# Kernel tuning notes

Measured on AMD Instinct MI355X. Metric: run time of the kernel, lower is better.

The kernel has to match this reference:

```python
import jax, jax.numpy as jnp
import numpy as np

D_MODEL = 1024
N_LAYER = 4
VOCAB = 50288  # 50277 padded to multiple of 16
D_STATE = 128
D_CONV = 4
HEADDIM = 64
CHUNK = 64
D_INNER = 2 * D_MODEL            # expand=2 -> 2048
NHEADS = D_INNER // HEADDIM      # 32
D_IN_PROJ = 2 * D_INNER + 2 * D_STATE + NHEADS  # ngroups=1
CONV_DIM = D_INNER + 2 * D_STATE
BATCH = 1
SEQLEN = 1024
EPS = 1e-5


def silu(x):
    return x * jax.nn.sigmoid(x)


def rmsnorm(x, w, z=None):
    if z is not None:
        x = x * silu(z)
    return x * jax.lax.rsqrt(jnp.mean(x * x, axis=-1, keepdims=True) + EPS) * w


def segsum(x):
    # x: (..., T) -> (..., T, T) with segment sums below diagonal, -inf above
    T = x.shape[-1]
    xe = jnp.broadcast_to(x[..., None], x.shape + (T,))
    mask_lo = jnp.tril(jnp.ones((T, T), dtype=bool), -1)
    xe = jnp.where(mask_lo, xe, 0.0)
    s = jnp.cumsum(xe, axis=-2)
    mask = jnp.tril(jnp.ones((T, T), dtype=bool), 0)
    return jnp.where(mask, s, -jnp.inf)


def ssd(x, dt, A, B, C, Dp):
    # x: (b,s,h,p), dt/A-broadcast: (b,s,h), B/C: (b,s,n) (ngroups=1), Dp: (h,)
    b, s = x.shape[0], x.shape[1]
    nchunks = s // CHUNK
    xD = x * Dp[:, None]
    Adt = A * dt                      # (b,s,h)
    xdt = x * dt[..., None]
    xr = xdt.reshape(b, nchunks, CHUNK, NHEADS, HEADDIM)
    Ar = Adt.reshape(b, nchunks, CHUNK, NHEADS).transpose(0, 3, 1, 2)  # (b,h,c,l)
    Br = B.reshape(b, nchunks, CHUNK, D_STATE)
    Cr = C.reshape(b, nchunks, CHUNK, D_STATE)
    A_cumsum = jnp.cumsum(Ar, axis=-1)                  # (b,h,c,l)
    L = jnp.exp(segsum(Ar))                             # (b,h,c,l,l)
    Y_diag = jnp.einsum('bcln,bcsn,bhcls,bcshp->bclhp', Cr, Br, L, xr)
    decay_states = jnp.exp(A_cumsum[..., -1:] - A_cumsum)
    states = jnp.einsum('bcln,bhcl,bclhp->bchpn', Br, decay_states, xr)
    states = jnp.concatenate([jnp.zeros_like(states[:, :1]), states], axis=1)
    decay_chunk = jnp.exp(segsum(jnp.pad(A_cumsum[..., -1], ((0, 0), (0, 0), (1, 0)))))
    new_states = jnp.einsum('bhzc,bchpn->bzhpn', decay_chunk, states)
    states = new_states[:, :-1]
    state_decay_out = jnp.exp(A_cumsum)
    Y_off = jnp.einsum('bcln,bchpn,bhcl->bclhp', Cr, states, state_decay_out)
    Y = (Y_diag + Y_off).reshape(b, s, NHEADS, HEADDIM) + xD
    return Y


def mamba2_forward(input_ids, embedding, norm_w, in_proj_w, conv_w, conv_b,
                   dt_bias, A_log, D, mixer_norm_w, out_proj_w, norm_f_w):
    h = embedding[input_ids]  # (b,s,d_model)
    for l in range(N_LAYER):
        u = rmsnorm(h, norm_w[l])
        zxbcdt = u @ in_proj_w[l].T  # (b,s,d_in_proj)
        z = zxbcdt[..., :D_INNER]
        xBC = zxbcdt[..., D_INNER:D_INNER + CONV_DIM]
        dt = jax.nn.softplus(zxbcdt[..., -NHEADS:] + dt_bias[l])
        # causal depthwise conv1d
        xc = jnp.transpose(xBC, (0, 2, 1))
        xc = jax.lax.conv_general_dilated(
            xc, conv_w[l], (1,), [(D_CONV - 1, 0)],
            dimension_numbers=('NCH', 'OIH', 'NCH'),
            feature_group_count=CONV_DIM) + conv_b[l][None, :, None]
        xBC = silu(jnp.transpose(xc, (0, 2, 1)))
        x = xBC[..., :D_INNER].reshape(BATCH, SEQLEN, NHEADS, HEADDIM)
        B = xBC[..., D_INNER:D_INNER + D_STATE]
        C = xBC[..., D_INNER + D_STATE:]
        A = -jnp.exp(A_log[l])  # (h,)
        y = ssd(x, dt, A, B, C, D[l])
        y = rmsnorm(y.reshape(BATCH, SEQLEN, D_INNER), mixer_norm_w[l], z)
        h = h + y @ out_proj_w[l].T
    h = rmsnorm(h, norm_f_w)
    return h @ embedding.T  # tied lm_head


def setup_inputs() -> dict:
    key = jax.random.key(0)
    ks = jax.random.split(key, 10)
    def rn(k, shape, s=0.02):
        return jax.random.normal(k, shape, jnp.float32) * s
    return {
        'input_ids': jax.random.randint(ks[0], (BATCH, SEQLEN), 0, VOCAB, jnp.int32),
        'embedding': rn(ks[1], (VOCAB, D_MODEL)),
        'norm_w': jnp.ones((N_LAYER, D_MODEL), jnp.float32),
        'in_proj_w': rn(ks[2], (N_LAYER, D_IN_PROJ, D_MODEL)),
        'conv_w': rn(ks[3], (N_LAYER, CONV_DIM, 1, D_CONV), 0.2),
        'conv_b': jnp.zeros((N_LAYER, CONV_DIM), jnp.float32),
        'dt_bias': rn(ks[4], (N_LAYER, NHEADS), 0.5),
        'A_log': jnp.log(jax.random.uniform(ks[5], (N_LAYER, NHEADS), jnp.float32, 1.0, 16.0)),
        'D': jnp.ones((N_LAYER, NHEADS), jnp.float32) + rn(ks[6], (N_LAYER, NHEADS), 0.1),
        'mixer_norm_w': jnp.ones((N_LAYER, D_INNER), jnp.float32),
        'out_proj_w': rn(ks[7], (N_LAYER, D_MODEL, D_INNER)),
        'norm_f_w': jnp.ones((D_MODEL,), jnp.float32),
    }


def reference(input_ids, embedding, norm_w, in_proj_w, conv_w, conv_b,
              dt_bias, A_log, D, mixer_norm_w, out_proj_w, norm_f_w):
    return mamba2_forward(input_ids, embedding, norm_w, in_proj_w, conv_w, conv_b,
                          dt_bias, A_log, D, mixer_norm_w, out_proj_w, norm_f_w)
```

## Files before the change

### kernel.cpp

```cpp
#include <hip/hip_runtime.h>
#include <hip/hip_bf16.h>
#include <math.h>

#define D_MODEL   1024
#define VOCAB     50288
#define D_STATE   128
#define D_CONV    4
#define HEADDIM   64
#define CHUNK     64
#define D_INNER   2048
#define NHEADS    32
#define D_IN_PROJ 4384
#define CONV_DIM  2304
#define SEQ       1024
#define NCHUNKS   16
#define EPS       1e-5f
#define SZH       1048576

typedef __bf16 bf16x8 __attribute__((ext_vector_type(8)));
typedef __bf16 bf16x4 __attribute__((ext_vector_type(4)));
typedef float  f32x4  __attribute__((ext_vector_type(4)));

__device__ __forceinline__ float blockReduceSum256(float v, float* sm) {
    #pragma unroll
    for (int off = 32; off > 0; off >>= 1) v += __shfl_down(v, off);
    if ((threadIdx.x & 63) == 0) sm[threadIdx.x >> 6] = v;
    __syncthreads();
    return sm[0] + sm[1] + sm[2] + sm[3];
}

__device__ __forceinline__ float sigmoidf_(float x) { return 1.0f / (1.0f + expf(-x)); }

__device__ __forceinline__ void gload_lds16(const __bf16* g, __bf16* l) {
    __builtin_amdgcn_global_load_lds(
        (const __attribute__((address_space(1))) void*)g,
        (__attribute__((address_space(3))) void*)l,
        16, 0, 0);
}

__global__ void cvt_bf16_k(const float* __restrict__ src, __bf16* __restrict__ dst, long n) {
    long i = ((long)blockIdx.x * 256 + threadIdx.x) * 8;
    long stride = (long)gridDim.x * 256 * 8;
    for (; i < n; i += stride) {
        float4 a = *(const float4*)(src + i);
        float4 b = *(const float4*)(src + i + 4);
        bf16x8 o;
        o[0] = (__bf16)a.x; o[1] = (__bf16)a.y; o[2] = (__bf16)a.z; o[3] = (__bf16)a.w;
        o[4] = (__bf16)b.x; o[5] = (__bf16)b.y; o[6] = (__bf16)b.z; o[7] = (__bf16)b.w;
        *(bf16x8*)(dst + i) = o;
    }
}

__global__ void gather_k(const int* __restrict__ ids, const float* __restrict__ emb,
                         float* __restrict__ h) {
    int s = blockIdx.x;
    int id = ids[s];
    const float4* src = (const float4*)(emb + (size_t)id * D_MODEL);
    float4* dst = (float4*)(h + (size_t)s * D_MODEL);
    dst[threadIdx.x] = src[threadIdx.x];
}

__global__ void rmsnorm_k(const float* __restrict__ x, const float* __restrict__ w,
                          float* __restrict__ o) {
    __shared__ float red[4];
    int s = blockIdx.x, t = threadIdx.x;
    float4 v = ((const float4*)(x + (size_t)s * D_MODEL))[t];
    float ss = v.x*v.x + v.y*v.y + v.z*v.z + v.w*v.w;
    float tot = blockReduceSum256(ss, red);
    float r = rsqrtf(tot / (float)D_MODEL + EPS);
    float4 wv = ((const float4*)w)[t];
    float4 ov;
    ov.x = v.x * r * wv.x; ov.y = v.y * r * wv.y;
    ov.z = v.z * r * wv.z; ov.w = v.w * r * wv.w;
    ((float4*)(o + (size_t)s * D_MODEL))[t] = ov;
}

__global__ void rmsnorm_fold_bf16_k(float* __restrict__ h, const float* __restrict__ o,
                                    const float* __restrict__ w, __bf16* __restrict__ out) {
    __shared__ float red[4];
    int s = blockIdx.x, t = threadIdx.x;
    float4 v = ((const float4*)(h + (size_t)s * D_MODEL))[t];
    if (o) {
        #pragma unroll
        for (int j = 0; j < 4; ++j) {
            float4 ov = ((const float4*)(o + (size_t)j * SZH + (size_t)s * D_MODEL))[t];
            v.x += ov.x; v.y += ov.y; v.z += ov.z; v.w += ov.w;
        }
        ((float4*)(h + (size_t)s * D_MODEL))[t] = v;
    }
    float ss = v.x*v.x + v.y*v.y + v.z*v.z + v.w*v.w;
    float tot = blockReduceSum256(ss, red);
    float r = rsqrtf(tot / (float)D_MODEL + EPS);
    float4 wv = ((const float4*)w)[t];
    bf16x4 ov;
    ov[0] = (__bf16)(v.x * r * wv.x); ov[1] = (__bf16)(v.y * r * wv.y);
    ov[2] = (__bf16)(v.z * r * wv.z); ov[3] = (__bf16)(v.w * r * wv.w);
    *(bf16x4*)(out + (size_t)s * D_MODEL + t * 4) = ov;
}

__global__ void gatednorm_k(float* __restrict__ Y, const float* __restrict__ zx,
                            const float* __restrict__ w) {
    __shared__ float red[4];
    int s = blockIdx.x, t = threadIdx.x;
    float4 y0 = ((const float4*)(Y + (size_t)s * D_INNER))[2*t];
    float4 y1 = ((const float4*)(Y + (size_t)s * D_INNER))[2*t+1];
    float4 z0 = ((const float4*)(zx + (size_t)s * D_IN_PROJ))[2*t];
    float4 z1 = ((const float4*)(zx + (size_t)s * D_IN_PROJ))[2*t+1];
    float g[8];
    float yv[8] = { y0.x,y0.y,y0.z,y0.w, y1.x,y1.y,y1.z,y1.w };
    float zv[8] = { z0.x,z0.y,z0.z,z0.w, z1.x,z1.y,z1.z,z1.w };
    float ss = 0.f;
    #pragma unroll
    for (int j = 0; j < 8; ++j) {
        float gg = yv[j] * zv[j] * sigmoidf_(zv[j]);
        g[j] = gg;
        ss += gg * gg;
    }
    float tot = blockReduceSum256(ss, red);
    float r = rsqrtf(tot / (float)D_INNER + EPS);
    float4 o0, o1;
    o0.x = g[0]*r*w[8*t+0]; o0.y = g[1]*r*w[8*t+1]; o0.z = g[2]*r*w[8*t+2]; o0.w = g[3]*r*w[8*t+3];
    o1.x = g[4]*r*w[8*t+4]; o1.y = g[5]*r*w[8*t+5]; o1.z = g[6]*r*w[8*t+6]; o1.w = g[7]*r*w[8*t+7];
    ((float4*)(Y + (size_t)s * D_INNER))[2*t]   = o0;
    ((float4*)(Y + (size_t)s * D_INNER))[2*t+1] = o1;
}

__global__ void gatednorm_bf16_k(const float* __restrict__ Y, const float* __restrict__ zx0,
                                 const float* __restrict__ zx1,
                                 const float* __restrict__ w, __bf16* __restrict__ o) {
    __shared__ float red[4];
    int s = blockIdx.x, t = threadIdx.x;
    float4 y0 = ((const float4*)(Y + (size_t)s * D_INNER))[2*t];
    float4 y1 = ((const float4*)(Y + (size_t)s * D_INNER))[2*t+1];
    float4 z0 = ((const float4*)(zx0 + (size_t)s * D_IN_PROJ))[2*t];
    float4 z1 = ((const float4*)(zx0 + (size_t)s * D_IN_PROJ))[2*t+1];
    if (zx1) {
        float4 a0 = ((const float4*)(zx1 + (size_t)s * D_IN_PROJ))[2*t];
        float4 a1 = ((const float4*)(zx1 + (size_t)s * D_IN_PROJ))[2*t+1];
        z0.x += a0.x; z0.y += a0.y; z0.z += a0.z; z0.w += a0.w;
        z1.x += a1.x; z1.y += a1.y; z1.z += a1.z; z1.w += a1.w;
    }
    float g[8];
    float yv[8] = { y0.x,y0.y,y0.z,y0.w, y1.x,y1.y,y1.z,y1.w };
    float zv[8] = { z0.x,z0.y,z0.z,z0.w, z1.x,z1.y,z1.z,z1.w };
    float ss = 0.f;
    #pragma unroll
    for (int j = 0; j < 8; ++j) {
        float gg = yv[j] * zv[j] * sigmoidf_(zv[j]);
        g[j] = gg;
        ss += gg * gg;
    }
    float tot = blockReduceSum256(ss, red);
    float r = rsqrtf(tot / (float)D_INNER + EPS);
    bf16x8 ov;
    #pragma unroll
    for (int j = 0; j < 8; ++j) ov[j] = (__bf16)(g[j] * r * w[8*t+j]);
    *(bf16x8*)(o + (size_t)s * D_INNER + t * 8) = ov;
}

template<int TM, int TN, int MTL2, bool ACC>
__global__ __launch_bounds__(256) void gemm_bt_bf16(const __bf16* __restrict__ A,
                                                    const __bf16* __restrict__ B,
                                                    float* __restrict__ C,
                                                    int N, int klen,
                                                    int lda, int ldb, int ldc,
                                                    int ntiles, size_t csplit) {
    constexpr int FM = TM / 32;
    constexpr int FN = TN / 32;
    __shared__ __bf16 As[TM * 32];
    __shared__ __bf16 Bs[TN * 32];

    const int d = blockIdx.x;
    const int xcd = d & 7;
    const int kk = d >> 3;
    const int p = kk >> MTL2;
    const int m_tile = kk & ((1 << MTL2) - 1);
    const int n_tile = xcd + (p << 3);
    if (n_tile >= ntiles) return;

    const int k_begin = blockIdx.y * klen;
    C += (size_t)blockIdx.y * csplit;

    const int bm0 = m_tile * TM;
    const int bn0 = n_tile * TN;
    const int t = threadIdx.x;
    const int l = t & 63;
    const int w = t >> 6;
    const int wr = w >> 1, wc = w & 1;
    const int lrow = l & 15;
    const int lk   = (l >> 4) * 8;
    const int srow = l >> 2;
    const int scol = (l & 3) * 8;

    f32x4 acc[FM][FN];
    #pragma unroll
    for (int m = 0; m < FM; ++m)
        #pragma unroll
        for (int n = 0; n < FN; ++n)
            acc[m][n] = (f32x4){0.f, 0.f, 0.f, 0.f};

    for (int k0 = k_begin; k0 < k_begin + klen; k0 += 32) {
        __syncthreads();
        #pragma unroll
        for (int i = 0; i < TM / 64; ++i) {
            int r0 = w * (TM / 4) + i * 16;
            const __bf16* g = A + (size_t)(bm0 + r0 + srow) * lda + k0 + scol;
            gload_lds16(g, As + (size_t)r0 * 32);
        }
        #pragma unroll
        for (int i = 0; i < TN / 64; ++i) {
            int r0 = w * (TN / 4) + i * 16;
            int gn = bn0 + r0 + srow; if (gn > N - 1) gn = N - 1;
            const __bf16* g = B + (size_t)gn * ldb + k0 + scol;
            gload_lds16(g, Bs + (size_t)r0 * 32);
        }
        __syncthreads();

        bf16x8 af[FM], bfr[FN];
        #pragma unroll
        for (int m = 0; m < FM; ++m)
            af[m] = *(const bf16x8*)&As[(wr * (TM/2) + m * 16 + lrow) * 32 + lk];
        #pragma unroll
        for (int n = 0; n < FN; ++n)
            bfr[n] = *(const bf16x8*)&Bs[(wc * (TN/2) + n * 16 + lrow) * 32 + lk];
        #pragma unroll
        for (int m = 0; m < FM; ++m)
            #pragma unroll
            for (int n = 0; n < FN; ++n)
                acc[m][n] = __builtin_amdgcn_mfma_f32_16x16x32_bf16(af[m], bfr[n], acc[m][n], 0, 0, 0);
    }

    const int r0 = (l >> 4) * 4;
    #pragma unroll
    for (int m = 0; m < FM; ++m) {
        #pragma unroll
        for (int rr = 0; rr < 4; ++rr) {
            int gr = bm0 + wr * (TM/2) + m * 16 + r0 + rr;
            #pragma unroll
            for (int n = 0; n < FN; ++n) {
                int gc = bn0 + wc * (TN/2) + n * 16 + lrow;
                if (gc < N) {
                    size_t off = (size_t)gr * ldc + gc;
                    if (ACC) C[off] += acc[m][n][rr];
                    else     C[off]  = acc[m][n][rr];
                }
            }
        }
    }
}

template<bool ACC>
__global__ __launch_bounds__(256) void gemm_nt_cvt(const float* __restrict__ A,
                                                   const float* __restrict__ B,
                                                   float* __restrict__ C,
                                                   int M, int N, int K,
                                                   int lda, int ldb, int ldc) {
    __shared__ __bf16 As[128][40];
    __shared__ __bf16 Bs[128][40];
    const int bm0 = blockIdx.x * 128;
    const int bn0 = blockIdx.y * 128;
    const int t = threadIdx.x;
    const int l = t & 63;
    const int w = t >> 6;
    const int wr = w >> 1;
    const int wc = w & 1;
    const int lrow = l & 15;
    const int lk   = (l >> 4) * 8;

    f32x4 acc[4][4];
    #pragma unroll
    for (int m = 0; m < 4; ++m)
        #pragma unroll
        for (int n = 0; n < 4; ++n)
            acc[m][n] = (f32x4){0.f, 0.f, 0.f, 0.f};

    for (int k0 = 0; k0 < K; k0 += 32) {
        __syncthreads();
        float4 av[4], bv[4];
        #pragma unroll
        for (int i = 0; i < 4; ++i) {
            int idx = t + i * 256;
            int r = idx >> 3;
            int c4 = (idx & 7) * 4;
            av[i] = *(const float4*)(A + (size_t)(bm0 + r) * lda + k0 + c4);
            int gn = bn0 + r; if (gn > N - 1) gn = N - 1;
            bv[i] = *(const float4*)(B + (size_t)gn * ldb + k0 + c4);
        }
        #pragma unroll
        for (int i = 0; i < 4; ++i) {
            int idx = t + i * 256;
            int r = idx >> 3;
            int c4 = (idx & 7) * 4;
            bf16x4 aw, bw;
            aw[0] = (__bf16)av[i].x; aw[1] = (__bf16)av[i].y;
            aw[2] = (__bf16)av[i].z; aw[3] = (__bf16)av[i].w;
            bw[0] = (__bf16)bv[i].x; bw[1] = (__bf16)bv[i].y;
            bw[2] = (__bf16)bv[i].z; bw[3] = (__bf16)bv[i].w;
            *(bf16x4*)&As[r][c4] = aw;
            *(bf16x4*)&Bs[r][c4] = bw;
        }
        __syncthreads();

        bf16x8 af[4], bfr[4];
        #pragma unroll
        for (int m = 0; m < 4; ++m)
            af[m] = *(const bf16x8*)&As[wr * 64 + m * 16 + lrow][lk];
        #pragma unroll
        for (int n = 0; n < 4; ++n)
            bfr[n] = *(const bf16x8*)&Bs[wc * 64 + n * 16 + lrow][lk];
        #pragma unroll
        for (int m = 0; m < 4; ++m)
            #pragma unroll
            for (int n = 0; n < 4; ++n)
                acc[m][n] = __builtin_amdgcn_mfma_f32_16x16x32_bf16(af[m], bfr[n], acc[m][n], 0, 0, 0);
    }

    const int r0 = (l >> 4) * 4;
    #pragma unroll
    for (int m = 0; m < 4; ++m) {
        #pragma unroll
        for (int rr = 0; rr < 4; ++rr) {
            int gr = bm0 + wr * 64 + m * 16 + r0 + rr;
            #pragma unroll
            for (int n = 0; n < 4; ++n) {
                int gc = bn0 + wc * 64 + n * 16 + lrow;
                if (gc < N) {
                    size_t off = (size_t)gr * ldc + gc;
                    if (ACC) C[off] += acc[m][n][rr];
                    else     C[off]  = acc[m][n][rr];
                }
            }
        }
    }
}

__global__ void conv_silu_k(const float* __restrict__ zx0, const float* __restrict__ zx1,
                            const float* __restrict__ w,
                            const float* __restrict__ b, float* __restrict__ xBC) {
    int idx = blockIdx.x * 256 + threadIdx.x;
    if (idx >= SEQ * CONV_DIM) return;
    int s = idx / CONV_DIM, c = idx - s * CONV_DIM;
    float acc = b[c];
    #pragma unroll
    for (int k = 0; k < D_CONV; ++k) {
        int si = s + k - (D_CONV - 1);
        if (si >= 0) {
            size_t o = (size_t)si * D_IN_PROJ + D_INNER + c;
            float v = zx0[o];
            if (zx1) v += zx1[o];
            acc = fmaf(v, w[c * D_CONV + k], acc);
        }
    }
    xBC[idx] = acc * sigmoidf_(acc);
}

__global__ void dtcum_k(const float* __restrict__ zx0, const float* __restrict__ zx1,
                        const float* __restrict__ dt_bias,
                        const float* __restrict__ A_log,
                        float* __restrict__ dtb, float* __restrict__ acs) {
    int c = blockIdx.x, h = blockIdx.y, l = threadIdx.x;
    int s = c * 64 + l;
    size_t o = (size_t)s * D_IN_PROJ + (D_IN_PROJ - NHEADS) + h;
    float v = zx0[o];
    if (zx1) v += zx1[o];
    v += dt_bias[h];
    float dt = (v > 20.f) ? v : log1pf(expf(v));
    dtb[(size_t)s * NHEADS + h] = dt;
    float a = -expf(A_log[h]);
    float x = a * dt;
    #pragma unroll
    for (int off = 1; off < 64; off <<= 1) {
        float oo = __shfl_up(x, off);
        if (l >= off) x += oo;
    }
    acs[(size_t)h * SEQ + s] = x;
}

__global__ __launch_bounds__(256) void chunk_cm_k(const float* __restrict__ xBC,
                                                  float* __restrict__ cm) {
    int c = blockIdx.x, g = blockIdx.y;
    __shared__ float Cs[16][D_STATE];
    __shared__ float BsT[D_STATE][64];
    int t = threadIdx.x;
    #pragma unroll
    for (int i = 0; i < 2; ++i) {
        int idx = t + i * 256;
        int li = idx >> 5, n4 = (idx & 31) * 4;
        *(float4*)&Cs[li][n4] =
            *(const float4*)(xBC + (size_t)(c*64 + g*16 + li) * CONV_DIM + D_INNER + D_STATE + n4);
    }
    #pragma unroll
    for (int i = 0; i < 8; ++i) {
        int idx = t + i * 256;
        int sx = idx & 63, n4 = (idx >> 6) * 4;
        float4 v = *(const float4*)(xBC + (size_t)(c*64 + sx) * CONV_DIM + D_INNER + n4);
        BsT[n4+0][sx] = v.x; BsT[n4+1][sx] = v.y; BsT[n4+2][sx] = v.z; BsT[n4+3][sx] = v.w;
    }
    __syncthreads();
    #pragma unroll
    for (int i = 0; i < 4; ++i) {
        int e = t + i * 256;
        int li = e >> 6, sx = e & 63;
        int l = g * 16 + li;
        float d = 0.f;
        if (sx <= l) {
            #pragma unroll 8
            for (int n = 0; n < D_STATE; ++n) d = fmaf(Cs[li][n], BsT[n][sx], d);
        }
        cm[(size_t)c * 4096 + l * 64 + sx] = d;
    }
}

__global__ __launch_bounds__(256) void ydst_k(const float* __restrict__ cm,
                                              const float* __restrict__ xBC,
                                              const float* __restrict__ dtb,
                                              const float* __restrict__ acs,
                                              float* __restrict__ Y,
                                              float* __restrict__ st) {
    int c = blockIdx.x, h = blockIdx.y;
    __shared__ float Xs[64][64];
    __shared__ float Us[64][128];
    __shared__ float arow[64];
    __shared__ float dec[64];
    int t = threadIdx.x;
    if (t < 64) arow[t] = acs[(size_t)h * SEQ + c * 64 + t];
    __syncthreads();
    float alast = arow[63];
    if (t < 64) dec[t] = expf(alast - arow[t]);
    #pragma unroll
    for (int i = 0; i < 4; ++i) {
        int idx = t + i * 256;
        int l = idx >> 4, p4 = (idx & 15) * 4;
        int s = c * 64 + l;
        float4 v = *(const float4*)(xBC + (size_t)s * CONV_DIM + h * HEADDIM + p4);
        float d = dtb[(size_t)s * NHEADS + h];
        v.x *= d; v.y *= d; v.z *= d; v.w *= d;
        *(float4*)&Xs[l][p4] = v;
    }
    #pragma unroll
    for (int i = 0; i < 16; ++i) {
        int e = t + i * 256;
        int l = e >> 6, sx = e & 63;
        Us[l][sx] = (sx <= l) ? cm[(size_t)c * 4096 + e] * expf(arow[l] - arow[sx]) : 0.f;
    }
    __syncthreads();
    #pragma unroll
    for (int i = 0; i < 4; ++i) {
        int e = t + i * 256;
        int l = e >> 4, p4 = (e & 15) * 4;
        float ax = 0.f, ay = 0.f, az = 0.f, aw = 0.f;
        for (int sx = 0; sx <= l; ++sx) {
            float gg = Us[l][sx];
            float4 xv = *(const float4*)&Xs[sx][p4];
            ax = fmaf(gg, xv.x, ax); ay = fmaf(gg, xv.y, ay);
            az = fmaf(gg, xv.z, az); aw = fmaf(gg, xv.w, aw);
        }
        float4 ov; ov.x = ax; ov.y = ay; ov.z = az; ov.w = aw;
        *(float4*)(Y + (size_t)(c*64 + l) * D_INNER + h * HEADDIM + p4) = ov;
    }
    __syncthreads();
    #pragma unroll
    for (int i = 0; i < 8; ++i) {
        int idx = t + i * 256;
        int l = idx >> 5, n4 = (idx & 31) * 4;
        *(float4*)&Us[l][n4] =
            *(const float4*)(xBC + (size_t)(c*64 + l) * CONV_DIM + D_INNER + n4);
    }
    __syncthreads();
    #pragma unroll
    for (int i = 0; i < 8; ++i) {
        int e = t + i * 256;
        int n = e >> 4, p4 = (e & 15) * 4;
        float ax = 0.f, ay = 0.f, az = 0.f, aw = 0.f;
        #pragma unroll 4
        for (int l = 0; l < 64; ++l) {
            float bd = Us[l][n] * dec[l];
            float4 xv = *(const float4*)&Xs[l][p4];
            ax = fmaf(bd, xv.x, ax); ay = fmaf(bd, xv.y, ay);
            az = fmaf(bd, xv.z, az); aw = fmaf(bd, xv.w, aw);
        }
        float4 ov; ov.x = ax; ov.y = ay; ov.z = az; ov.w = aw;
        *(float4*)(st + ((size_t)(c * NHEADS + h) * D_STATE + n) * HEADDIM + p4) = ov;
    }
}

__global__ void rec_k(float* __restrict__ st, const float* __restrict__ acs) {
    int idx = blockIdx.x * 256 + threadIdx.x;
    int h = idx >> 13;
    float S = 0.f;
    for (int c = 0; c < NCHUNKS; ++c) {
        float* p = st + (size_t)c * (NHEADS * D_STATE * HEADDIM) + idx;
        float tmp = *p;
        *p = S;
        float dec = expf(acs[(size_t)h * SEQ + c * 64 + 63]);
        S = fmaf(S, dec, tmp);
    }
}

__global__ __launch_bounds__(256) void yoff_k(const float* __restrict__ xBC,
                                              const float* __restrict__ acs,
                                              const float* __restrict__ st,
                                              const float* __restrict__ Dp,
                                              float* __restrict__ Y) {
    int c = blockIdx.x, h = blockIdx.y;
    __shared__ float Cs[64][D_STATE];
    __shared__ float Ss[D_STATE][64];
    __shared__ float arow[64];
    int t = threadIdx.x;
    if (t < 64) arow[t] = acs[(size_t)h * SEQ + c * 64 + t];
    #pragma unroll
    for (int i = 0; i < 8; ++i) {
        int idx = t + i * 256;
        int l = idx >> 5, n4 = (idx & 31) * 4;
        *(float4*)&Cs[l][n4] =
            *(const float4*)(xBC + (size_t)(c*64 + l) * CONV_DIM + D_INNER + D_STATE + n4);
    }
    #pragma unroll
    for (int i = 0; i < 8; ++i) {
        int idx = t + i * 256;
        int n = idx >> 4, p4 = (idx & 15) * 4;
        *(float4*)&Ss[n][p4] =
            *(const float4*)(st + ((size_t)(c * NHEADS + h) * D_STATE + n) * HEADDIM + p4);
    }
    __syncthreads();
    float dpar = Dp[h];
    #pragma unroll
    for (int i = 0; i < 4; ++i) {
        int e = t + i * 256;
        int l = e >> 4, p4 = (e & 15) * 4;
        float ax = 0.f, ay = 0.f, az = 0.f, aw = 0.f;
        #pragma unroll 4
        for (int n = 0; n < D_STATE; ++n) {
            float cc = Cs[l][n];
            float4 sv = *(const float4*)&Ss[n][p4];
            ax = fmaf(cc, sv.x, ax); ay = fmaf(cc, sv.y, ay);
            az = fmaf(cc, sv.z, az); aw = fmaf(cc, sv.w, aw);
        }
        float sc = expf(arow[l]);
        int s = c * 64 + l;
        float4 xv = *(const float4*)(xBC + (size_t)s * CONV_DIM + h * HEADDIM + p4);
        float4 yv = *(float4*)(Y + (size_t)s * D_INNER + h * HEADDIM + p4);
        yv.x += sc * ax + dpar * xv.x;
        yv.y += sc * ay + dpar * xv.y;
        yv.z += sc * az + dpar * xv.z;
        yv.w += sc * aw + dpar * xv.w;
        *(float4*)(Y + (size_t)s * D_INNER + h * HEADDIM + p4) = yv;
    }
}

extern "C" void kernel_launch(void* const* d_in, const int* in_sizes, int n_in,
                              void* d_out, int out_size, void* d_ws, size_t ws_size,
                              hipStream_t stream) {
    const int*   ids          = (const int*)d_in[0];
    const float* emb          = (const float*)d_in[1];
    const float* norm_w       = (const float*)d_in[2];
    const float* in_proj_w    = (const float*)d_in[3];
    const float* conv_w       = (const float*)d_in[4];
    const float* conv_b       = (const float*)d_in[5];
    const float* dt_bias      = (const float*)d_in[6];
    const float* A_log        = (const float*)d_in[7];
    const float* Dp           = (const float*)d_in[8];
    const float* mixer_norm_w = (const float*)d_in[9];
    const float* out_proj_w   = (const float*)d_in[10];
    const float* norm_f_w     = (const float*)d_in[11];
    float* out = (float*)d_out;

    const size_t SZ_H = SZH, SZ_U = SZH, SZ_ZX = 4489216, SZ_XBC = 2359296,
                 SZ_DT = 32768, SZ_ACS = 32768, SZ_CM = 65536, SZ_ST = 4194304, SZ_Y = 2097152;
    const size_t BF_U = SZ_H, BF_Y = SZ_Y;
    const size_t BF_WIN  = 4ull * 4489216;
    const size_t BF_WOUT = 4ull * 2097152;
    const size_t BF_EMB  = (size_t)VOCAB * D_MODEL;

    const size_t f32_base = SZ_H + SZ_U + SZ_ZX + SZ_XBC + SZ_DT + SZ_ACS + SZ_CM + SZ_ST + SZ_Y;
    const size_t f32_new  = f32_base + SZ_ZX + 4 * SZ_H;
    const size_t bf_all   = (BF_U + BF_Y + BF_WIN + BF_WOUT + BF_EMB) * 2;
    const size_t bytesNew = f32_new * 4 + bf_all;
    const size_t bytesOld = f32_base * 4 + bf_all;
    const int tier = (ws_size >= bytesNew) ? 0 : (ws_size >= bytesOld) ? 1 : 2;

    float *h, *u, *dtb, *acs, *cm, *zx, *zxb = nullptr, *xBC, *st, *Y, *o = nullptr;
    __bf16 *ub = nullptr, *Yb = nullptr, *win = nullptr, *wout = nullptr, *embb = nullptr;

    if (tier <= 1) {
        float* f = (float*)d_ws;
        h = f;   f += SZ_H;
        u = f;   f += SZ_U;
        dtb = f; f += SZ_DT;
        acs = f; f += SZ_ACS;
        cm = f;  f += SZ_CM;
        zx = f;  f += SZ_ZX;
        if (tier == 0) {
            zxb = f; f += SZ_ZX;
            o = f;   f += 4 * SZ_H;
        }
        xBC = f; f += SZ_XBC;
        st = f;  f += SZ_ST;
        Y = f;   f += SZ_Y;
        __bf16* bb = (__bf16*)f;
        ub = bb;   bb += BF_U;
        Yb = bb;   bb += BF_Y;
        win = bb;  bb += BF_WIN;
        wout = bb; bb += BF_WOUT;
        embb = bb;
    } else {
        float* f = (float*)d_ws;
        h = f;   f += SZ_H;
        u = f;   f += SZ_U;
        dtb = f; f += SZ_DT;
        acs = f; f += SZ_ACS;
        cm = f;  f += SZ_CM;
        float* ob = (float*)d_out;
        zx = ob;
        xBC = zx + SZ_ZX;
        st = xBC + SZ_XBC;
        Y = st + SZ_ST;
    }

    if (tier <= 1) {
        cvt_bf16_k<<<(int)(BF_WIN / 2048), 256, 0, stream>>>(in_proj_w, win, (long)BF_WIN);
        cvt_bf16_k<<<(int)(BF_WOUT / 2048), 256, 0, stream>>>(out_proj_w, wout, (long)BF_WOUT);
        cvt_bf16_k<<<(int)(BF_EMB / 2048), 256, 0, stream>>>(emb, embb, (long)BF_EMB);
    }

    gather_k<<<SEQ, 256, 0, stream>>>(ids, emb, h);

    const int NT_IN  = (D_IN_PROJ + 127) / 128;
    const int NT_OUT = D_MODEL / 128;
    const int NT_LM  = (VOCAB + 127) / 128;
    const int GX_IN  = 8 * ((NT_IN  + 7) / 8) * 8;
    const int GX_OUT = 8 * ((NT_OUT + 7) / 8) * 16;
    const int GX_LM  = 8 * ((NT_LM  + 7) / 8) * 8;

    for (int l = 0; l < 4; ++l) {
        if (tier <= 1) {
            rmsnorm_fold_bf16_k<<<SEQ, 256, 0, stream>>>(
                h, (tier == 0 && l > 0) ? o : nullptr, norm_w + (size_t)l * D_MODEL, ub);
            if (tier == 0) {
                gemm_bt_bf16<128, 128, 3, false><<<dim3(GX_IN, 2), 256, 0, stream>>>(
                    ub, win + (size_t)l * 4489216, zx,
                    D_IN_PROJ, 512, D_MODEL, D_MODEL, D_IN_PROJ, NT_IN, SZ_ZX);
            } else {
                gemm_bt_bf16<128, 128, 3, false><<<dim3(GX_IN, 1), 256, 0, stream>>>(
                    ub, win + (size_t)l * 4489216, zx,
                    D_IN_PROJ, 1024, D_MODEL, D_MODEL, D_IN_PROJ, NT_IN, 0);
            }
        } else {
            rmsnorm_k<<<SEQ, 256, 0, stream>>>(h, norm_w + (size_t)l * D_MODEL, u);
            gemm_nt_cvt<false><<<dim3(8, 35), 256, 0, stream>>>(
                u, in_proj_w + (size_t)l * D_IN_PROJ * D_MODEL, zx,
                SEQ, D_IN_PROJ, D_MODEL, D_MODEL, D_MODEL, D_IN_PROJ);
        }

        float* zx1 = (tier == 0) ? zxb : nullptr;

        conv_silu_k<<<(SEQ * CONV_DIM) / 256, 256, 0, stream>>>(
            zx, zx1, conv_w + (size_t)l * CONV_DIM * D_CONV, conv_b + (size_t)l * CONV_DIM, xBC);

        dtcum_k<<<dim3(NCHUNKS, NHEADS), 64, 0, stream>>>(
            zx, zx1, dt_bias + (size_t)l * NHEADS, A_log + (size_t)l * NHEADS, dtb, acs);

        chunk_cm_k<<<dim3(NCHUNKS, 4), 256, 0, stream>>>(xBC, cm);

        ydst_k<<<dim3(NCHUNKS, NHEADS), 256, 0, stream>>>(cm, xBC, dtb, acs, Y, st);

        rec_k<<<(NHEADS * D_STATE * HEADDIM) / 256, 256, 0, stream>>>(st, acs);

        yoff_k<<<dim3(NCHUNKS, NHEADS), 256, 0, stream>>>(xBC, acs, st, Dp + (size_t)l * NHEADS, Y);

        if (tier <= 1) {
            gatednorm_bf16_k<<<SEQ, 256, 0, stream>>>(Y, zx, zx1, mixer_norm_w + (size_t)l * D_INNER, Yb);
            if (tier == 0) {
                gemm_bt_bf16<64, 128, 4, false><<<dim3(GX_OUT, 4), 256, 0, stream>>>(
                    Yb, wout + (size_t)l * 2097152, o,
                    D_MODEL, 512, D_INNER, D_INNER, D_MODEL, NT_OUT, SZ_H);
            } else {
                gemm_bt_bf16<64, 128, 4, true><<<dim3(GX_OUT, 1), 256, 0, stream>>>(
                    Yb, wout + (size_t)l * 2097152, h,
                    D_MODEL, 2048, D_INNER, D_INNER, D_MODEL, NT_OUT, 0);
            }
        } else {
            gatednorm_k<<<SEQ, 256, 0, stream>>>(Y, zx, mixer_norm_w + (size_t)l * D_INNER);
            gemm_nt_cvt<true><<<dim3(8, 8), 256, 0, stream>>>(
                Y, out_proj_w + (size_t)l * D_MODEL * D_INNER, h,
                SEQ, D_MODEL, D_INNER, D_INNER, D_INNER, D_MODEL);
        }
    }

    if (tier <= 1) {
        rmsnorm_fold_bf16_k<<<SEQ, 256, 0, stream>>>(
            h, (tier == 0) ? o : nullptr, norm_f_w, ub);
        gemm_bt_bf16<128, 128, 3, false><<<dim3(GX_LM, 1), 256, 0, stream>>>(
            ub, embb, out, VOCAB, 1024, D_MODEL, D_MODEL, VOCAB, NT_LM, 0);
    } else {
        rmsnorm_k<<<SEQ, 256, 0, stream>>>(h, norm_f_w, u);
        gemm_nt_cvt<false><<<dim3(8, (VOCAB + 127) / 128), 256, 0, stream>>>(
            u, emb, out, SEQ, VOCAB, D_MODEL, D_MODEL, D_MODEL, VOCAB);
    }
}
```

Before: 826.6 us.

## Move SSD chunk matmuls to bf16 MFMA with pre-transposed B buffer

Rewrites the chunk C·B^T, intra-chunk Y_diag, chunk-state and Y_off computations to use 16x16x32 bf16 MFMA instructions instead of scalar fp32 FMA loops. The B operand is converted to bf16 and transposed once per chunk into a new global buffer that the per-head kernel reuses. The decay factor is folded into a second scaled copy of x, and the state layout changes to (p, n) order. This cuts the scalar FMA work in these kernels but adds bf16 rounding in the SSD path and a new workspace buffer.

```diff
diff --git a/kernel.cpp b/kernel.cpp
--- a/kernel.cpp
+++ b/kernel.cpp
@@ -376,111 +376,162 @@
     acs[(size_t)h * SEQ + s] = x;
 }
 
-__global__ __launch_bounds__(256) void chunk_cm_k(const float* __restrict__ xBC,
-                                                  float* __restrict__ cm) {
-    int c = blockIdx.x, g = blockIdx.y;
-    __shared__ float Cs[16][D_STATE];
-    __shared__ float BsT[D_STATE][64];
-    int t = threadIdx.x;
-    #pragma unroll
-    for (int i = 0; i < 2; ++i) {
-        int idx = t + i * 256;
-        int li = idx >> 5, n4 = (idx & 31) * 4;
-        *(float4*)&Cs[li][n4] =
-            *(const float4*)(xBC + (size_t)(c*64 + g*16 + li) * CONV_DIM + D_INNER + D_STATE + n4);
-    }
+__global__ __launch_bounds__(256) void cmg_k(const float* __restrict__ xBC,
+                                             float* __restrict__ cm,
+                                             __bf16* __restrict__ btg) {
+    const int c = blockIdx.x;
+    const int LDP = 136;
+    __shared__ __bf16 Cs[64 * 136];
+    __shared__ __bf16 Bs[64 * 136];
+    const int t = threadIdx.x;
+    const int l = t & 63;
+    const int w = t >> 6;
+
     #pragma unroll
     for (int i = 0; i < 8; ++i) {
-        int idx = t + i * 256;
-        int sx = idx & 63, n4 = (idx >> 6) * 4;
-        float4 v = *(const float4*)(xBC + (size_t)(c*64 + sx) * CONV_DIM + D_INNER + n4);
-        BsT[n4+0][sx] = v.x; BsT[n4+1][sx] = v.y; BsT[n4+2][sx] = v.z; BsT[n4+3][sx] = v.w;
+        int e = t + i * 256;
+        int row = e >> 5, n4 = (e & 31) * 4;
+        float4 vc = *(const float4*)(xBC + (size_t)(c*64 + row) * CONV_DIM + D_INNER + D_STATE + n4);
+        float4 vb = *(const float4*)(xBC + (size_t)(c*64 + row) * CONV_DIM + D_INNER + n4);
+        bf16x4 cc, bb;
+        cc[0] = (__bf16)vc.x; cc[1] = (__bf16)vc.y; cc[2] = (__bf16)vc.z; cc[3] = (__bf16)vc.w;
+        bb[0] = (__bf16)vb.x; bb[1] = (__bf16)vb.y; bb[2] = (__bf16)vb.z; bb[3] = (__bf16)vb.w;
+        *(bf16x4*)&Cs[row * LDP + n4] = cc;
+        *(bf16x4*)&Bs[row * LDP + n4] = bb;
     }
     __syncthreads();
+
     #pragma unroll
     for (int i = 0; i < 4; ++i) {
-        int e = t + i * 256;
-        int li = e >> 6, sx = e & 63;
-        int l = g * 16 + li;
-        float d = 0.f;
-        if (sx <= l) {
-            #pragma unroll 8
-            for (int n = 0; n < D_STATE; ++n) d = fmaf(Cs[li][n], BsT[n][sx], d);
-        }
-        cm[(size_t)c * 4096 + l * 64 + sx] = d;
-    }
+        int e8 = t + i * 256;
+        int n = e8 >> 3, l8 = (e8 & 7) * 8;
+        bf16x8 o;
+        #pragma unroll
+        for (int j = 0; j < 8; ++j) o[j] = Bs[(l8 + j) * LDP + n];
+        *(bf16x8*)(btg + ((size_t)c * 128 + n) * 64 + l8) = o;
+    }
+
+    const int lrow = l & 15;
+    const int lk   = (l >> 4) * 8;
+    const int l0 = w * 16;
+    f32x4 acc[4];
+    #pragma unroll
+    for (int n = 0; n < 4; ++n) acc[n] = (f32x4){0.f,0.f,0.f,0.f};
+    #pragma unroll
+    for (int kc = 0; kc < 4; ++kc) {
+        bf16x8 a = *(const bf16x8*)&Cs[(l0 + lrow) * LDP + kc * 32 + lk];
+        #pragma unroll
+        for (int n = 0; n < 4; ++n) {
+            bf16x8 b = *(const bf16x8*)&Bs[(n * 16 + lrow) * LDP + kc * 32 + lk];
+            acc[n] = __builtin_amdgcn_mfma_f32_16x16x32_bf16(a, b, acc[n], 0, 0, 0);
+        }
+    }
+    const int r0 = (l >> 4) * 4;
+    #pragma unroll
+    for (int n = 0; n < 4; ++n)
+        #pragma unroll
+        for (int r = 0; r < 4; ++r)
+            cm[(size_t)c * 4096 + (l0 + r0 + r) * 64 + n * 16 + lrow] = acc[n][r];
 }
 
 __global__ __launch_bounds__(256) void ydst_k(const float* __restrict__ cm,
+                                              const __bf16* __restrict__ btg,
                                               const float* __restrict__ xBC,
                                               const float* __restrict__ dtb,
                                               const float* __restrict__ acs,
                                               float* __restrict__ Y,
                                               float* __restrict__ st) {
-    int c = blockIdx.x, h = blockIdx.y;
-    __shared__ float Xs[64][64];
-    __shared__ float Us[64][128];
+    const int c = blockIdx.x, h = blockIdx.y;
+    const int LDP = 72;
+    __shared__ __bf16 Xt[64 * 72];
+    __shared__ __bf16 X2[64 * 72];
+    __shared__ __bf16 G [64 * 72];
+    __shared__ __bf16 Bt[128 * 72];
     __shared__ float arow[64];
-    __shared__ float dec[64];
-    int t = threadIdx.x;
+    __shared__ float decl[64];
+    const int t = threadIdx.x;
+    const int l = t & 63;
+    const int w = t >> 6;
+
     if (t < 64) arow[t] = acs[(size_t)h * SEQ + c * 64 + t];
     __syncthreads();
-    float alast = arow[63];
-    if (t < 64) dec[t] = expf(alast - arow[t]);
+    const float alast = arow[63];
+    if (t < 64) decl[t] = expf(alast - arow[t]);
+    #pragma unroll
+    for (int i = 0; i < 16; ++i) {
+        int e = t + i * 256;
+        int gl = e >> 6, sx = e & 63;
+        G[gl * LDP + sx] = (sx <= gl) ? (__bf16)(cm[(size_t)c * 4096 + e] * expf(arow[gl] - arow[sx])) : (__bf16)0.f;
+    }
     #pragma unroll
     for (int i = 0; i < 4; ++i) {
-        int idx = t + i * 256;
-        int l = idx >> 4, p4 = (idx & 15) * 4;
-        int s = c * 64 + l;
+        int e8 = t + i * 256;
+        int n = e8 >> 3, l8 = (e8 & 7) * 8;
+        *(bf16x8*)&Bt[n * LDP + l8] = *(const bf16x8*)(btg + ((size_t)c * 128 + n) * 64 + l8);
+    }
+    __syncthreads();
+    #pragma unroll
+    for (int i = 0; i < 4; ++i) {
+        int e4 = t + i * 256;
+        int sx = e4 >> 4, p4 = (e4 & 15) * 4;
+        int s = c * 64 + sx;
         float4 v = *(const float4*)(xBC + (size_t)s * CONV_DIM + h * HEADDIM + p4);
         float d = dtb[(size_t)s * NHEADS + h];
-        v.x *= d; v.y *= d; v.z *= d; v.w *= d;
-        *(float4*)&Xs[l][p4] = v;
-    }
-    #pragma unroll
-    for (int i = 0; i < 16; ++i) {
-        int e = t + i * 256;
-        int l = e >> 6, sx = e & 63;
-        Us[l][sx] = (sx <= l) ? cm[(size_t)c * 4096 + e] * expf(arow[l] - arow[sx]) : 0.f;
+        float d2 = d * decl[sx];
+        Xt[(p4+0) * LDP + sx] = (__bf16)(v.x * d);
+        Xt[(p4+1) * LDP + sx] = (__bf16)(v.y * d);
+        Xt[(p4+2) * LDP + sx] = (__bf16)(v.z * d);
+        Xt[(p4+3) * LDP + sx] = (__bf16)(v.w * d);
+        X2[(p4+0) * LDP + sx] = (__bf16)(v.x * d2);
+        X2[(p4+1) * LDP + sx] = (__bf16)(v.y * d2);
+        X2[(p4+2) * LDP + sx] = (__bf16)(v.z * d2);
+        X2[(p4+3) * LDP + sx] = (__bf16)(v.w * d2);
     }
     __syncthreads();
-    #pragma unroll
-    for (int i = 0; i < 4; ++i) {
-        int e = t + i * 256;
-        int l = e >> 4, p4 = (e & 15) * 4;
-        float ax = 0.f, ay = 0.f, az = 0.f, aw = 0.f;
-        for (int sx = 0; sx <= l; ++sx) {
-            float gg = Us[l][sx];
-            float4 xv = *(const float4*)&Xs[sx][p4];
-            ax = fmaf(gg, xv.x, ax); ay = fmaf(gg, xv.y, ay);
-            az = fmaf(gg, xv.z, az); aw = fmaf(gg, xv.w, aw);
-        }
-        float4 ov; ov.x = ax; ov.y = ay; ov.z = az; ov.w = aw;
-        *(float4*)(Y + (size_t)(c*64 + l) * D_INNER + h * HEADDIM + p4) = ov;
-    }
-    __syncthreads();
-    #pragma unroll
-    for (int i = 0; i < 8; ++i) {
-        int idx = t + i * 256;
-        int l = idx >> 5, n4 = (idx & 31) * 4;
-        *(float4*)&Us[l][n4] =
-            *(const float4*)(xBC + (size_t)(c*64 + l) * CONV_DIM + D_INNER + n4);
-    }
-    __syncthreads();
-    #pragma unroll
-    for (int i = 0; i < 8; ++i) {
-        int e = t + i * 256;
-        int n = e >> 4, p4 = (e & 15) * 4;
-        float ax = 0.f, ay = 0.f, az = 0.f, aw = 0.f;
-        #pragma unroll 4
-        for (int l = 0; l < 64; ++l) {
-            float bd = Us[l][n] * dec[l];
-            float4 xv = *(const float4*)&Xs[l][p4];
-            ax = fmaf(bd, xv.x, ax); ay = fmaf(bd, xv.y, ay);
-            az = fmaf(bd, xv.z, az); aw = fmaf(bd, xv.w, aw);
-        }
-        float4 ov; ov.x = ax; ov.y = ay; ov.z = az; ov.w = aw;
-        *(float4*)(st + ((size_t)(c * NHEADS + h) * D_STATE + n) * HEADDIM + p4) = ov;
+
+    const int lrow = l & 15;
+    const int lk   = (l >> 4) * 8;
+    const int p0 = w * 16;
+    const int r0 = (l >> 4) * 4;
+
+    f32x4 acc1[4];
+    #pragma unroll
+    for (int n = 0; n < 4; ++n) acc1[n] = (f32x4){0.f,0.f,0.f,0.f};
+    #pragma unroll
+    for (int kc = 0; kc < 2; ++kc) {
+        bf16x8 a = *(const bf16x8*)&Xt[(p0 + lrow) * LDP + kc * 32 + lk];
+        #pragma unroll
+        for (int n = 0; n < 4; ++n) {
+            bf16x8 b = *(const bf16x8*)&G[(n * 16 + lrow) * LDP + kc * 32 + lk];
+            acc1[n] = __builtin_amdgcn_mfma_f32_16x16x32_bf16(a, b, acc1[n], 0, 0, 0);
+        }
+    }
+    #pragma unroll
+    for (int n = 0; n < 4; ++n) {
+        int lc = n * 16 + lrow;
+        float4 ov; ov.x = acc1[n][0]; ov.y = acc1[n][1]; ov.z = acc1[n][2]; ov.w = acc1[n][3];
+        *(float4*)(Y + (size_t)(c*64 + lc) * D_INNER + h * HEADDIM + p0 + r0) = ov;
+    }
+
+    f32x4 acc2[8];
+    #pragma unroll
+    for (int n = 0; n < 8; ++n) acc2[n] = (f32x4){0.f,0.f,0.f,0.f};
+    #pragma unroll
+    for (int kc = 0; kc < 2; ++kc) {
+        bf16x8 a = *(const bf16x8*)&X2[(p0 + lrow) * LDP + kc * 32 + lk];
+        #pragma unroll
+        for (int n = 0; n < 8; ++n) {
+            bf16x8 b = *(const bf16x8*)&Bt[(n * 16 + lrow) * LDP + kc * 32 + lk];
+            acc2[n] = __builtin_amdgcn_mfma_f32_16x16x32_bf16(a, b, acc2[n], 0, 0, 0);
+        }
+    }
+    float* stb = st + ((size_t)(c * NHEADS + h) * 64) * 128;
+    #pragma unroll
+    for (int n = 0; n < 8; ++n) {
+        int nc = n * 16 + lrow;
+        #pragma unroll
+        for (int r = 0; r < 4; ++r)
+            stb[(size_t)(p0 + r0 + r) * 128 + nc] = acc2[n][r];
     }
 }
 
@@ -502,49 +553,61 @@
                                               const float* __restrict__ st,
                                               const float* __restrict__ Dp,
                                               float* __restrict__ Y) {
-    int c = blockIdx.x, h = blockIdx.y;
-    __shared__ float Cs[64][D_STATE];
-    __shared__ float Ss[D_STATE][64];
+    const int c = blockIdx.x, h = blockIdx.y;
+    const int LDP = 136;
+    __shared__ __bf16 Sts[64 * 136];
+    __shared__ __bf16 Cs [64 * 136];
     __shared__ float arow[64];
-    int t = threadIdx.x;
+    const int t = threadIdx.x;
+    const int l = t & 63;
+    const int w = t >> 6;
+
     if (t < 64) arow[t] = acs[(size_t)h * SEQ + c * 64 + t];
+    const float* stb = st + ((size_t)(c * NHEADS + h) * 64) * 128;
     #pragma unroll
     for (int i = 0; i < 8; ++i) {
-        int idx = t + i * 256;
-        int l = idx >> 5, n4 = (idx & 31) * 4;
-        *(float4*)&Cs[l][n4] =
-            *(const float4*)(xBC + (size_t)(c*64 + l) * CONV_DIM + D_INNER + D_STATE + n4);
-    }
-    #pragma unroll
-    for (int i = 0; i < 8; ++i) {
-        int idx = t + i * 256;
-        int n = idx >> 4, p4 = (idx & 15) * 4;
-        *(float4*)&Ss[n][p4] =
-            *(const float4*)(st + ((size_t)(c * NHEADS + h) * D_STATE + n) * HEADDIM + p4);
+        int e = t + i * 256;
+        int row = e >> 5, n4 = (e & 31) * 4;
+        float4 vs = *(const float4*)(stb + (size_t)row * 128 + n4);
+        float4 vc = *(const float4*)(xBC + (size_t)(c*64 + row) * CONV_DIM + D_INNER + D_STATE + n4);
+        bf16x4 ss, cc;
+        ss[0] = (__bf16)vs.x; ss[1] = (__bf16)vs.y; ss[2] = (__bf16)vs.z; ss[3] = (__bf16)vs.w;
+        cc[0] = (__bf16)vc.x; cc[1] = (__bf16)vc.y; cc[2] = (__bf16)vc.z; cc[3] = (__bf16)vc.w;
+        *(bf16x4*)&Sts[row * LDP + n4] = ss;
+        *(bf16x4*)&Cs [row * LDP + n4] = cc;
     }
     __syncthreads();
-    float dpar = Dp[h];
-    #pragma unroll
-    for (int i = 0; i < 4; ++i) {
-        int e = t + i * 256;
-        int l = e >> 4, p4 = (e & 15) * 4;
-        float ax = 0.f, ay = 0.f, az = 0.f, aw = 0.f;
-        #pragma unroll 4
-        for (int n = 0; n < D_STATE; ++n) {
-            float cc = Cs[l][n];
-            float4 sv = *(const float4*)&Ss[n][p4];
-            ax = fmaf(cc, sv.x, ax); ay = fmaf(cc, sv.y, ay);
-            az = fmaf(cc, sv.z, az); aw = fmaf(cc, sv.w, aw);
-        }
-        float sc = expf(arow[l]);
-        int s = c * 64 + l;
-        float4 xv = *(const float4*)(xBC + (size_t)s * CONV_DIM + h * HEADDIM + p4);
-        float4 yv = *(float4*)(Y + (size_t)s * D_INNER + h * HEADDIM + p4);
-        yv.x += sc * ax + dpar * xv.x;
-        yv.y += sc * ay + dpar * xv.y;
-        yv.z += sc * az + dpar * xv.z;
-        yv.w += sc * aw + dpar * xv.w;
-        *(float4*)(Y + (size_t)s * D_INNER + h * HEADDIM + p4) = yv;
+
+    const int lrow = l & 15;
+    const int lk   = (l >> 4) * 8;
+    const int p0 = w * 16;
+    const int r0 = (l >> 4) * 4;
+    const float dpar = Dp[h];
+
+    f32x4 acc[4];
+    #pragma unroll
+    for (int n = 0; n < 4; ++n) acc[n] = (f32x4){0.f,0.f,0.f,0.f};
+    #pragma unroll
+    for (int kc = 0; kc < 4; ++kc) {
+        bf16x8 a = *(const bf16x8*)&Sts[(p0 + lrow) * LDP + kc * 32 + lk];
+        #pragma unroll
+        for (int n = 0; n < 4; ++n) {
+            bf16x8 b = *(const bf16x8*)&Cs[(n * 16 + lrow) * LDP + kc * 32 + lk];
+            acc[n] = __builtin_amdgcn_mfma_f32_16x16x32_bf16(a, b, acc[n], 0, 0, 0);
+        }
+    }
+    #pragma unroll
+    for (int n = 0; n < 4; ++n) {
+        int lc = n * 16 + lrow;
+        int s = c * 64 + lc;
+        float sc = expf(arow[lc]);
+        float4 xv = *(const float4*)(xBC + (size_t)s * CONV_DIM + h * HEADDIM + p0 + r0);
+        float4 yv = *(float4*)(Y + (size_t)s * D_INNER + h * HEADDIM + p0 + r0);
+        yv.x += sc * acc[n][0] + dpar * xv.x;
+        yv.y += sc * acc[n][1] + dpar * xv.y;
+        yv.z += sc * acc[n][2] + dpar * xv.z;
+        yv.w += sc * acc[n][3] + dpar * xv.w;
+        *(float4*)(Y + (size_t)s * D_INNER + h * HEADDIM + p0 + r0) = yv;
     }
 }
 
@@ -567,12 +630,13 @@
 
     const size_t SZ_H = SZH, SZ_U = SZH, SZ_ZX = 4489216, SZ_XBC = 2359296,
                  SZ_DT = 32768, SZ_ACS = 32768, SZ_CM = 65536, SZ_ST = 4194304, SZ_Y = 2097152;
+    const size_t SZ_BTG_F = 65536;
     const size_t BF_U = SZ_H, BF_Y = SZ_Y;
     const size_t BF_WIN  = 4ull * 4489216;
     const size_t BF_WOUT = 4ull * 2097152;
     const size_t BF_EMB  = (size_t)VOCAB * D_MODEL;
 
-    const size_t f32_base = SZ_H + SZ_U + SZ_ZX + SZ_XBC + SZ_DT + SZ_ACS + SZ_CM + SZ_ST + SZ_Y;
+    const size_t f32_base = SZ_H + SZ_U + SZ_ZX + SZ_XBC + SZ_DT + SZ_ACS + SZ_CM + SZ_BTG_F + SZ_ST + SZ_Y;
     const size_t f32_new  = f32_base + SZ_ZX + 4 * SZ_H;
     const size_t bf_all   = (BF_U + BF_Y + BF_WIN + BF_WOUT + BF_EMB) * 2;
     const size_t bytesNew = f32_new * 4 + bf_all;
@@ -580,7 +644,7 @@
     const int tier = (ws_size >= bytesNew) ? 0 : (ws_size >= bytesOld) ? 1 : 2;
 
     float *h, *u, *dtb, *acs, *cm, *zx, *zxb = nullptr, *xBC, *st, *Y, *o = nullptr;
-    __bf16 *ub = nullptr, *Yb = nullptr, *win = nullptr, *wout = nullptr, *embb = nullptr;
+    __bf16 *btg, *ub = nullptr, *Yb = nullptr, *win = nullptr, *wout = nullptr, *embb = nullptr;
 
     if (tier <= 1) {
         float* f = (float*)d_ws;
@@ -589,6 +653,7 @@
         dtb = f; f += SZ_DT;
         acs = f; f += SZ_ACS;
         cm = f;  f += SZ_CM;
+        btg = (__bf16*)f; f += SZ_BTG_F;
         zx = f;  f += SZ_ZX;
         if (tier == 0) {
             zxb = f; f += SZ_ZX;
@@ -610,6 +675,7 @@
         dtb = f; f += SZ_DT;
         acs = f; f += SZ_ACS;
         cm = f;  f += SZ_CM;
+        btg = (__bf16*)f; f += SZ_BTG_F;
         float* ob = (float*)d_out;
         zx = ob;
         xBC = zx + SZ_ZX;
@@ -660,9 +726,9 @@
         dtcum_k<<<dim3(NCHUNKS, NHEADS), 64, 0, stream>>>(
             zx, zx1, dt_bias + (size_t)l * NHEADS, A_log + (size_t)l * NHEADS, dtb, acs);
 
-        chunk_cm_k<<<dim3(NCHUNKS, 4), 256, 0, stream>>>(xBC, cm);
-
-        ydst_k<<<dim3(NCHUNKS, NHEADS), 256, 0, stream>>>(cm, xBC, dtb, acs, Y, st);
+        cmg_k<<<NCHUNKS, 256, 0, stream>>>(xBC, cm, btg);
+
+        ydst_k<<<dim3(NCHUNKS, NHEADS), 256, 0, stream>>>(cm, btg, xBC, dtb, acs, Y, st);
 
         rec_k<<<(NHEADS * D_STATE * HEADDIM) / 256, 256, 0, stream>>>(st, acs);
 
```

New measurement: 721.5 us. 12.7% less time.
